# Optimization experiments

Measured on AMD Instinct MI355X. Metric: run time of the kernel, lower is better.

Reference implementation:

```python
import jax, jax.numpy as jnp
import numpy as np

B, S, D = 4, 2048, 256   # batch, seq, d_output (= d_k = d_v here)
H = 8                    # num_head


def setup_inputs() -> dict:
    key = jax.random.key(0)
    ks = jax.random.split(key, 8)
    Q = jax.random.normal(ks[0], (B, S, D), dtype=jnp.float32)
    K = jax.random.normal(ks[1], (B, S, D), dtype=jnp.float32)
    V = jax.random.normal(ks[2], (B, S, D), dtype=jnp.float32)
    M = jax.random.uniform(ks[3], (B, S, S), dtype=jnp.float32)  # multiplicative mask
    # per-head projection weights, stacked over heads (truncated_normal ~ normal here)
    W_Q = jax.random.normal(ks[4], (H, D, D), dtype=jnp.float32) * 0.05
    W_K = jax.random.normal(ks[5], (H, D, D), dtype=jnp.float32) * 0.05
    W_V = jax.random.normal(ks[6], (H, D, D), dtype=jnp.float32) * 0.05
    W_mh = jax.random.normal(ks[7], (H * D, D), dtype=jnp.float32) * 0.05
    return {"Q": Q, "K": K, "V": V, "M": M,
            "W_Q": W_Q, "W_K": W_K, "W_V": W_V, "W_mh": W_mh}


def reference(Q, K, V, M, W_Q, W_K, W_V, W_mh):
    d_k = W_Q.shape[-1]
    scale = 1.0 / np.sqrt(d_k).astype(np.float32)
    # per-head projections, vectorized over heads
    Qh = jnp.einsum('bsd,hdk->bhsk', Q, W_Q)          # [B,H,S,dk]
    Kh = jnp.einsum('bsd,hdk->bhsk', K, W_K)          # [B,H,S,dk]
    Vh = jnp.einsum('bsd,hdv->bhsv', V, W_V)          # [B,H,S,dv]
    # scaled similarity with MULTIPLICATIVE mask applied before softmax
    scores = jnp.einsum('bhsk,bhtk->bhst', Qh, Kh) * scale * M[:, None]
    attn = jax.nn.softmax(scores, axis=-1)            # [B,H,S,S]
    heads = jnp.einsum('bhst,bhtv->bhsv', attn, Vh)   # [B,H,S,dv]
    # concat heads along feature dim: [B,S,H*dv]
    Bv, Hv, Sv, Dv = heads.shape
    heads = heads.transpose(0, 2, 1, 3).reshape(Bv, Sv, Hv * Dv)
    return heads @ W_mh                               # [B,S,d_output]
```

## Files before the change

kernel.cpp:

```cpp
#include <hip/hip_runtime.h>
#include <hip/hip_bf16.h>
#include <stdint.h>

#define B_ 4
#define S_ 2048
#define D_ 256
#define H_ 8

using f32x4  = __attribute__((ext_vector_type(4))) float;
using f32x16 = __attribute__((ext_vector_type(16))) float;
using bf16x4 = __attribute__((ext_vector_type(4))) __bf16;
using bf16x8 = __attribute__((ext_vector_type(8))) __bf16;

static __device__ __forceinline__ unsigned short f2bf(float x) {
    union { float f; unsigned u; } v; v.f = x;
    unsigned r = (v.u + 0x7FFFu + ((v.u >> 16) & 1u)) >> 16;
    return (unsigned short)r;
}

static __device__ __forceinline__ f32x4 mfma16(bf16x8 a, bf16x8 b, f32x4 c) {
    return __builtin_amdgcn_mfma_f32_16x16x32_bf16(a, b, c, 0, 0, 0);
}
static __device__ __forceinline__ f32x16 mfma32(bf16x8 a, bf16x8 b, f32x16 c) {
    return __builtin_amdgcn_mfma_f32_32x32x16_bf16(a, b, c, 0, 0, 0);
}

static __device__ __forceinline__ unsigned cvt_pk_bf16(float lo, float hi) {
    unsigned r;
    asm volatile("v_cvt_pk_bf16_f32 %0, %1, %2" : "=v"(r) : "v"(lo), "v"(hi));
    return r;
}

static __device__ __forceinline__ void gl_lds16(const void* g, void* l) {
    __builtin_amdgcn_global_load_lds((const __attribute__((address_space(1))) void*)g,
                                     (__attribute__((address_space(3))) void*)l, 16, 0, 0);
}
static __device__ __forceinline__ void gl_lds4(const void* g, void* l) {
    __builtin_amdgcn_global_load_lds((const __attribute__((address_space(1))) void*)g,
                                     (__attribute__((address_space(3))) void*)l, 4, 0, 0);
}

static __device__ __forceinline__ void drain_vmem_then_sync() {
    asm volatile("s_waitcnt vmcnt(0)" ::: "memory");
    __builtin_amdgcn_sched_barrier(0);
    __syncthreads();
}

__global__ __launch_bounds__(256) void wtrans_kernel(
        const float* __restrict__ Wq, const float* __restrict__ Wk,
        const float* __restrict__ Wv, const float* __restrict__ Wmh,
        unsigned short* __restrict__ WqkvT, unsigned short* __restrict__ WmhT) {
    int idx = blockIdx.x * 256 + threadIdx.x;
    const int NQKV = 3 * H_ * 256 * 256;
    if (idx < NQKV) {
        int d = idx & 255, n = (idx >> 8) & 255, h = (idx >> 16) & 7, which = idx >> 19;
        const float* W = (which == 0) ? Wq : ((which == 1) ? Wk : Wv);
        WqkvT[idx] = f2bf(W[(h * 256 + d) * 256 + n]);
    } else {
        int j = idx - NQKV;
        int k = j & 2047, n = j >> 11;
        WmhT[j] = f2bf(Wmh[k * 256 + n]);
    }
}

__global__ __launch_bounds__(256, 2) void proj_kernel(
        const float* __restrict__ Q, const float* __restrict__ K,
        const float* __restrict__ V, const unsigned short* __restrict__ WqkvT,
        unsigned short* __restrict__ Qh, unsigned short* __restrict__ Kh,
        unsigned short* __restrict__ VhT) {
    __shared__ __attribute__((aligned(16))) unsigned char smem[65536];
    int tid = threadIdx.x;
    int nt = blockIdx.x & 3, h = (blockIdx.x >> 2) & 7, which = blockIdx.x >> 5;
    int mt = blockIdx.y;
    const float* X = (which == 0) ? Q : ((which == 1) ? K : V);

    {
        const float4* Xv = (const float4*)(X + (size_t)mt * 64 * 256);
        #pragma unroll
        for (int j = 0; j < 16; ++j) {
            int c = tid + 256 * j;
            int row = c >> 6, c4 = c & 63;
            float4 x = Xv[c];
            ushort4 p;
            p.x = f2bf(x.x); p.y = f2bf(x.y); p.z = f2bf(x.z); p.w = f2bf(x.w);
            *(ushort4*)(smem + row * 512 + ((c4 * 8) ^ ((row & 7) << 4))) = p;
        }
    }
    {
        const uint4* Wv_ = (const uint4*)(WqkvT + (size_t)((which * H_ + h) * 256 + nt * 64) * 256);
        #pragma unroll
        for (int j = 0; j < 8; ++j) {
            int c = tid + 256 * j;
            int row = c >> 5, slot = c & 31;
            *(uint4*)(smem + 32768 + row * 512 + ((slot * 16) ^ ((row & 7) << 4))) = Wv_[c];
        }
    }
    __syncthreads();

    int w = tid >> 6, l = tid & 63, lr = l & 15, lg = l >> 4;
    f32x4 acc[4];
    #pragma unroll
    for (int fr = 0; fr < 4; ++fr) acc[fr] = (f32x4){0.f, 0.f, 0.f, 0.f};

    #pragma unroll
    for (int ks = 0; ks < 8; ++ks) {
        int arow = 16 * w + lr;
        bf16x8 a = *(const bf16x8*)(smem + arow * 512 + ((64 * ks + 16 * lg) ^ ((arow & 7) << 4)));
        #pragma unroll
        for (int fr = 0; fr < 4; ++fr) {
            int brow = 16 * fr + lr;
            bf16x8 b = *(const bf16x8*)(smem + 32768 + brow * 512 + ((64 * ks + 16 * lg) ^ ((brow & 7) << 4)));
            acc[fr] = mfma16(a, b, acc[fr]);
        }
    }

    int m0 = mt * 64 + 16 * w + 4 * lg;
    int b = m0 >> 11, s0 = m0 & 2047;
    if (which < 2) {
        unsigned short* out = (which == 0) ? Qh : Kh;
        float sc = (which == 0) ? 0.0625f : 1.0f;
        #pragma unroll
        for (int fr = 0; fr < 4; ++fr) {
            int n = nt * 64 + 16 * fr + lr;
            #pragma unroll
            for (int i = 0; i < 4; ++i)
                out[(size_t)((b * H_ + h) * S_ + s0 + i) * D_ + n] = f2bf(acc[fr][i] * sc);
        }
    } else {
        #pragma unroll
        for (int fr = 0; fr < 4; ++fr) {
            int n = nt * 64 + 16 * fr + lr;
            ushort4 p;
            p.x = f2bf(acc[fr][0]); p.y = f2bf(acc[fr][1]);
            p.z = f2bf(acc[fr][2]); p.w = f2bf(acc[fr][3]);
            *(ushort4*)(VhT + (size_t)((b * H_ + h) * D_ + n) * S_ + s0) = p;
        }
    }
}

__global__ __launch_bounds__(512, 2) void attn2_kernel(
        const unsigned short* Qh, const unsigned short* __restrict__ Kh,
        const unsigned short* __restrict__ VhT, const float* __restrict__ M,
        unsigned short* heads) {
    __shared__ __attribute__((aligned(16))) unsigned char smem[131072];
    const int tid = threadIdx.x;
    const int w = tid >> 6, l = tid & 63;
    const int qg = w >> 1, ts = w & 1;
    const int ql = l & 31, hi = l >> 5;

    int n = blockIdx.x;
    int x = n & 7, r0 = n >> 3;
    int h = r0 & 7, ghi = r0 >> 3;
    int g = x + 8 * ghi;
    int qt = g & 15, b = g >> 4;
    int bh = b * H_ + h;

    const unsigned short* KhP = Kh + (size_t)bh * S_ * D_;
    const unsigned short* VTP = VhT + (size_t)bh * D_ * S_;

    const int q = qt * 128 + qg * 32 + ql;
    const float* MrowP = M + (size_t)b * S_ * S_ + (size_t)q * S_;

    bf16x8 qf[16];
    {
        const unsigned short* QhP = Qh + ((size_t)bh * S_ + q) * D_;
        #pragma unroll
        for (int ks = 0; ks < 16; ++ks)
            qf[ks] = *(const bf16x8*)(QhP + ks * 16 + hi * 8);
    }

    f32x16 o[8];
    #pragma unroll
    for (int vb = 0; vb < 8; ++vb) o[vb] = (f32x16){};
    float mrun = -1e30f, lrun = 0.f;

    const int krow = ts * 32 + ql;
    const unsigned kbase = (unsigned)(krow * 512 + ((hi * 16) ^ ((krow & 15) << 5)));
    const unsigned vtbase = (unsigned)(ql * 128 + (((ts * 64) | (hi * 16)) ^ ((ql & 15) << 3)));

    const int ksr = 8 * w + (l >> 5);
    const unsigned kcol = (l & 31) * 16;
    const int vsr = 32 * w + (l >> 5);
    const unsigned vcol = (l & 31) * 4;

    int cur = 0;

    auto stage = [&](int tt, int bsel) {
        unsigned char* kb = smem + bsel * 32768;
        unsigned char* vb = smem + 65536 + bsel * 32768;
        #pragma unroll
        for (int j = 0; j < 4; ++j) {
            int row = ksr + 2 * j;
            const unsigned char* src = (const unsigned char*)KhP +
                (size_t)(tt * 64 + row) * 512 + (kcol ^ ((row & 15) << 5));
            gl_lds16(src, kb + (8 * w + 2 * j) * 512);
        }
        #pragma unroll
        for (int i = 0; i < 16; ++i) {
            int v = vsr + 2 * i;
            const unsigned char* src = (const unsigned char*)VTP +
                (size_t)v * (S_ * 2) + tt * 128 + (vcol ^ ((v & 15) << 3));
            gl_lds4(src, vb + (32 * w + 2 * i) * 128);
        }
    };

    stage(0, 0);
    drain_vmem_then_sync();

    #pragma unroll 1
    for (int tt = 0; tt < 32; ++tt) {
        stage((tt + 1) & 31, cur ^ 1);

        const unsigned char* kp = smem + cur * 32768;
        const unsigned char* vp = smem + 65536 + cur * 32768;

        const float* Mt = MrowP + tt * 64 + ts * 32 + 4 * hi;
        float4 mv0 = *(const float4*)(Mt);
        float4 mv1 = *(const float4*)(Mt + 8);
        float4 mv2 = *(const float4*)(Mt + 16);
        float4 mv3 = *(const float4*)(Mt + 24);

        f32x16 sacc = (f32x16){};
        #pragma unroll
        for (int ks = 0; ks < 16; ++ks) {
            bf16x8 a = *(const bf16x8*)(kp + (kbase ^ (unsigned)(ks * 32)));
            sacc = mfma32(a, qf[ks], sacc);
        }

        float p[16];
        #pragma unroll
        for (int rg = 0; rg < 4; ++rg) {
            float4 mv = (rg == 0) ? mv0 : (rg == 1) ? mv1 : (rg == 2) ? mv2 : mv3;
            #pragma unroll
            for (int j = 0; j < 4; ++j) p[4 * rg + j] = sacc[4 * rg + j] * ((const float*)&mv)[j];
        }

        float tm = p[0];
        #pragma unroll
        for (int i = 1; i < 16; ++i) tm = fmaxf(tm, p[i]);
        float tmm = fmaxf(tm, __shfl_xor(tm, 32, 64));

        if (__any(tmm > mrun)) {
            float nm = fmaxf(mrun, tmm);
            float f = __expf(mrun - nm);
            #pragma unroll
            for (int vb = 0; vb < 8; ++vb) o[vb] *= f;
            lrun *= f;
            mrun = nm;
        }

        float rs = 0.f;
        #pragma unroll
        for (int i = 0; i < 16; ++i) { p[i] = __expf(p[i] - mrun); rs += p[i]; }
        lrun += rs;

        unsigned own0 = cvt_pk_bf16(p[0], p[1]),  own1 = cvt_pk_bf16(p[2], p[3]);
        unsigned own2 = cvt_pk_bf16(p[4], p[5]),  own3 = cvt_pk_bf16(p[6], p[7]);
        unsigned own4 = cvt_pk_bf16(p[8], p[9]),  own5 = cvt_pk_bf16(p[10], p[11]);
        unsigned own6 = cvt_pk_bf16(p[12], p[13]), own7 = cvt_pk_bf16(p[14], p[15]);
        unsigned rec0 = __shfl_xor((int)own0, 32, 64), rec1 = __shfl_xor((int)own1, 32, 64);
        unsigned rec2 = __shfl_xor((int)own2, 32, 64), rec3 = __shfl_xor((int)own3, 32, 64);
        unsigned rec4 = __shfl_xor((int)own4, 32, 64), rec5 = __shfl_xor((int)own5, 32, 64);
        unsigned rec6 = __shfl_xor((int)own6, 32, 64), rec7 = __shfl_xor((int)own7, 32, 64);

        union { unsigned u[4]; bf16x8 v; } f0, f1;
        f0.u[0] = hi ? rec2 : own0;  f0.u[1] = hi ? rec3 : own1;
        f0.u[2] = hi ? own2 : rec0;  f0.u[3] = hi ? own3 : rec1;
        f1.u[0] = hi ? rec6 : own4;  f1.u[1] = hi ? rec7 : own5;
        f1.u[2] = hi ? own6 : rec4;  f1.u[3] = hi ? own7 : rec5;

        #pragma unroll
        for (int tstep = 0; tstep < 2; ++tstep) {
            bf16x8 pf = tstep ? f1.v : f0.v;
            unsigned a0 = vtbase ^ (unsigned)(tstep * 32);
            #pragma unroll
            for (int vb = 0; vb < 8; ++vb) {
                bf16x4 lo4 = *(const bf16x4*)(vp + vb * 4096 + a0);
                bf16x4 hi4 = *(const bf16x4*)(vp + vb * 4096 + (a0 ^ 8u));
                bf16x8 av = __builtin_shufflevector(lo4, hi4, 0, 1, 2, 3, 4, 5, 6, 7);
                o[vb] = mfma32(av, pf, o[vb]);
            }
        }

        drain_vmem_then_sync();
        cur ^= 1;
    }

    lrun += __shfl_xor(lrun, 32, 64);

    float2* mlb = (float2*)smem;
    if (hi == 0) mlb[(qg * 2 + ts) * 32 + ql] = make_float2(mrun, lrun);
    __syncthreads();
    float2 oth = mlb[(qg * 2 + (ts ^ 1)) * 32 + ql];
    __syncthreads();

    float mstar = fmaxf(mrun, oth.x);
    float aS = __expf(mrun - mstar), aO = __expf(oth.x - mstar);
    float inv = 1.f / (aS * lrun + aO * oth.y);
    float sc = aS * inv;
    #pragma unroll
    for (int vb = 0; vb < 8; ++vb) o[vb] *= sc;

    float* ob = (float*)smem;
    if (ts == 1) {
        #pragma unroll
        for (int vb = 0; vb < 8; ++vb)
            #pragma unroll
            for (int r = 0; r < 16; ++r) {
                int v = 32 * vb + (r & 3) + 8 * (r >> 2) + 4 * hi;
                ob[qg * 8192 + v * 32 + ql] = o[vb][r];
            }
    }
    __syncthreads();
    if (ts == 0) {
        unsigned short* hp = heads + ((size_t)bh * S_ + q) * D_;
        #pragma unroll
        for (int vb = 0; vb < 8; ++vb) {
            #pragma unroll
            for (int rg = 0; rg < 4; ++rg) {
                int v0 = 32 * vb + 8 * rg + 4 * hi;
                ushort4 pk;
                pk.x = f2bf(o[vb][4 * rg + 0] + ob[qg * 8192 + (v0 + 0) * 32 + ql]);
                pk.y = f2bf(o[vb][4 * rg + 1] + ob[qg * 8192 + (v0 + 1) * 32 + ql]);
                pk.z = f2bf(o[vb][4 * rg + 2] + ob[qg * 8192 + (v0 + 2) * 32 + ql]);
                pk.w = f2bf(o[vb][4 * rg + 3] + ob[qg * 8192 + (v0 + 3) * 32 + ql]);
                *(ushort4*)(hp + v0) = pk;
            }
        }
    }
}

__global__ __launch_bounds__(256, 2) void out_kernel(
        const unsigned short* __restrict__ heads,
        const unsigned short* __restrict__ WmhT, float* __restrict__ out) {
    __shared__ __attribute__((aligned(16))) unsigned char smem[65536];
    int tid = threadIdx.x;
    int nt = blockIdx.x, mt = blockIdx.y;
    int w = tid >> 6, l = tid & 63, lr = l & 15, lg = l >> 4;
    int m0 = mt * 64;
    int b = m0 >> 11, s00 = m0 & 2047;

    f32x4 acc[4];
    #pragma unroll
    for (int fr = 0; fr < 4; ++fr) acc[fr] = (f32x4){0.f, 0.f, 0.f, 0.f};

    for (int h = 0; h < H_; ++h) {
        __syncthreads();
        {
            const uint4* src = (const uint4*)(heads + (size_t)((b * H_ + h) * S_ + s00) * D_);
            #pragma unroll
            for (int j = 0; j < 8; ++j) {
                int c = tid + 256 * j;
                int row = c >> 5, slot = c & 31;
                *(uint4*)(smem + row * 512 + ((slot * 16) ^ ((row & 7) << 4))) = src[c];
            }
        }
        {
            #pragma unroll
            for (int j = 0; j < 8; ++j) {
                int c = tid + 256 * j;
                int row = c >> 5, slot = c & 31;
                uint4 xx = *(const uint4*)(WmhT + (size_t)(nt * 64 + row) * 2048 + h * 256 + slot * 8);
                *(uint4*)(smem + 32768 + row * 512 + ((slot * 16) ^ ((row & 7) << 4))) = xx;
            }
        }
        __syncthreads();
        #pragma unroll
        for (int ks = 0; ks < 8; ++ks) {
            int arow = 16 * w + lr;
            bf16x8 a = *(const bf16x8*)(smem + arow * 512 + ((64 * ks + 16 * lg) ^ ((arow & 7) << 4)));
            #pragma unroll
            for (int fr = 0; fr < 4; ++fr) {
                int brow = 16 * fr + lr;
                bf16x8 bb = *(const bf16x8*)(smem + 32768 + brow * 512 + ((64 * ks + 16 * lg) ^ ((brow & 7) << 4)));
                acc[fr] = mfma16(a, bb, acc[fr]);
            }
        }
    }

    int mrow = mt * 64 + 16 * w + 4 * lg;
    #pragma unroll
    for (int fr = 0; fr < 4; ++fr) {
        int nn = nt * 64 + 16 * fr + lr;
        #pragma unroll
        for (int i = 0; i < 4; ++i)
            out[(size_t)(mrow + i) * D_ + nn] = acc[fr][i];
    }
}

extern "C" void kernel_launch(void* const* d_in, const int* in_sizes, int n_in,
                              void* d_out, int out_size, void* d_ws, size_t ws_size,
                              hipStream_t stream) {
    const float* Q   = (const float*)d_in[0];
    const float* K   = (const float*)d_in[1];
    const float* V   = (const float*)d_in[2];
    const float* M   = (const float*)d_in[3];
    const float* Wq  = (const float*)d_in[4];
    const float* Wk  = (const float*)d_in[5];
    const float* Wv  = (const float*)d_in[6];
    const float* Wmh = (const float*)d_in[7];
    float* out = (float*)d_out;

    char* ws = (char*)d_ws;
    unsigned short* Qh    = (unsigned short*)(ws);
    unsigned short* Kh    = (unsigned short*)(ws + 33554432);
    unsigned short* VhT   = (unsigned short*)(ws + 67108864);
    unsigned short* WqkvT = (unsigned short*)(ws + 100663296);
    unsigned short* WmhT  = (unsigned short*)(ws + 103809024);

    wtrans_kernel<<<dim3(8192), dim3(256), 0, stream>>>(Wq, Wk, Wv, Wmh, WqkvT, WmhT);
    proj_kernel<<<dim3(96, 128), dim3(256), 0, stream>>>(Q, K, V, WqkvT, Qh, Kh, VhT);
    attn2_kernel<<<dim3(512), dim3(512), 0, stream>>>(Qh, Kh, VhT, M, Qh);
    out_kernel<<<dim3(4, 128), dim3(256), 0, stream>>>(Qh, WmhT, out);
}
```

Before: 644.0 us.

## Pre-convert mask to bf16, prefetch mask tiles, lazy softmax rescale, reorder blocks

```diff
diff --git a/kernel.cpp b/kernel.cpp
--- a/kernel.cpp
+++ b/kernel.cpp
@@ -16,6 +16,10 @@
     union { float f; unsigned u; } v; v.f = x;
     unsigned r = (v.u + 0x7FFFu + ((v.u >> 16) & 1u)) >> 16;
     return (unsigned short)r;
+}
+static __device__ __forceinline__ float bf2f(unsigned short u) {
+    union { unsigned u32; float f; } v; v.u32 = ((unsigned)u) << 16;
+    return v.f;
 }
 
 static __device__ __forceinline__ f32x4 mfma16(bf16x8 a, bf16x8 b, f32x4 c) {
@@ -63,6 +67,18 @@
     }
 }
 
+__global__ __launch_bounds__(256) void mconv_kernel(
+        const float* __restrict__ M, unsigned short* __restrict__ Mb) {
+    int i = (blockIdx.x * 256 + threadIdx.x) * 8;
+    float4 a = *(const float4*)(M + i);
+    float4 b = *(const float4*)(M + i + 4);
+    ushort4 lo, hi;
+    lo.x = f2bf(a.x); lo.y = f2bf(a.y); lo.z = f2bf(a.z); lo.w = f2bf(a.w);
+    hi.x = f2bf(b.x); hi.y = f2bf(b.y); hi.z = f2bf(b.z); hi.w = f2bf(b.w);
+    *(ushort4*)(Mb + i) = lo;
+    *(ushort4*)(Mb + i + 4) = hi;
+}
+
 __global__ __launch_bounds__(256, 2) void proj_kernel(
         const float* __restrict__ Q, const float* __restrict__ K,
         const float* __restrict__ V, const unsigned short* __restrict__ WqkvT,
@@ -138,10 +154,11 @@
     }
 }
 
+template <bool MB>
 __global__ __launch_bounds__(512, 2) void attn2_kernel(
         const unsigned short* Qh, const unsigned short* __restrict__ Kh,
         const unsigned short* __restrict__ VhT, const float* __restrict__ M,
-        unsigned short* heads) {
+        const unsigned short* __restrict__ Mb, unsigned short* heads) {
     __shared__ __attribute__((aligned(16))) unsigned char smem[131072];
     const int tid = threadIdx.x;
     const int w = tid >> 6, l = tid & 63;
@@ -149,17 +166,15 @@
     const int ql = l & 31, hi = l >> 5;
 
     int n = blockIdx.x;
-    int x = n & 7, r0 = n >> 3;
-    int h = r0 & 7, ghi = r0 >> 3;
-    int g = x + 8 * ghi;
-    int qt = g & 15, b = g >> 4;
+    int h = n & 7, qt = (n >> 3) & 15, b = n >> 7;
     int bh = b * H_ + h;
 
     const unsigned short* KhP = Kh + (size_t)bh * S_ * D_;
     const unsigned short* VTP = VhT + (size_t)bh * D_ * S_;
 
     const int q = qt * 128 + qg * 32 + ql;
-    const float* MrowP = M + (size_t)b * S_ * S_ + (size_t)q * S_;
+    const float* MP = M + (size_t)b * S_ * S_ + (size_t)q * S_;
+    const unsigned short* MbP = Mb + (size_t)b * S_ * S_ + (size_t)q * S_;
 
     bf16x8 qf[16];
     {
@@ -204,7 +219,26 @@
         }
     };
 
+    ushort4 mh0, mh1, mh2, mh3;
+    float4  mf0, mf1, mf2, mf3;
+    auto mload = [&](int tt) {
+        if constexpr (MB) {
+            const unsigned short* p = MbP + tt * 64 + ts * 32 + 4 * hi;
+            mh0 = *(const ushort4*)(p);
+            mh1 = *(const ushort4*)(p + 8);
+            mh2 = *(const ushort4*)(p + 16);
+            mh3 = *(const ushort4*)(p + 24);
+        } else {
+            const float* p = MP + tt * 64 + ts * 32 + 4 * hi;
+            mf0 = *(const float4*)(p);
+            mf1 = *(const float4*)(p + 8);
+            mf2 = *(const float4*)(p + 16);
+            mf3 = *(const float4*)(p + 24);
+        }
+    };
+
     stage(0, 0);
+    mload(0);
     drain_vmem_then_sync();
 
     #pragma unroll 1
@@ -214,12 +248,6 @@
         const unsigned char* kp = smem + cur * 32768;
         const unsigned char* vp = smem + 65536 + cur * 32768;
 
-        const float* Mt = MrowP + tt * 64 + ts * 32 + 4 * hi;
-        float4 mv0 = *(const float4*)(Mt);
-        float4 mv1 = *(const float4*)(Mt + 8);
-        float4 mv2 = *(const float4*)(Mt + 16);
-        float4 mv3 = *(const float4*)(Mt + 24);
-
         f32x16 sacc = (f32x16){};
         #pragma unroll
         for (int ks = 0; ks < 16; ++ks) {
@@ -228,19 +256,34 @@
         }
 
         float p[16];
-        #pragma unroll
-        for (int rg = 0; rg < 4; ++rg) {
-            float4 mv = (rg == 0) ? mv0 : (rg == 1) ? mv1 : (rg == 2) ? mv2 : mv3;
-            #pragma unroll
-            for (int j = 0; j < 4; ++j) p[4 * rg + j] = sacc[4 * rg + j] * ((const float*)&mv)[j];
-        }
+        if constexpr (MB) {
+            p[0]  = sacc[0]  * bf2f(mh0.x); p[1]  = sacc[1]  * bf2f(mh0.y);
+            p[2]  = sacc[2]  * bf2f(mh0.z); p[3]  = sacc[3]  * bf2f(mh0.w);
+            p[4]  = sacc[4]  * bf2f(mh1.x); p[5]  = sacc[5]  * bf2f(mh1.y);
+            p[6]  = sacc[6]  * bf2f(mh1.z); p[7]  = sacc[7]  * bf2f(mh1.w);
+            p[8]  = sacc[8]  * bf2f(mh2.x); p[9]  = sacc[9]  * bf2f(mh2.y);
+            p[10] = sacc[10] * bf2f(mh2.z); p[11] = sacc[11] * bf2f(mh2.w);
+            p[12] = sacc[12] * bf2f(mh3.x); p[13] = sacc[13] * bf2f(mh3.y);
+            p[14] = sacc[14] * bf2f(mh3.z); p[15] = sacc[15] * bf2f(mh3.w);
+        } else {
+            p[0]  = sacc[0]  * mf0.x; p[1]  = sacc[1]  * mf0.y;
+            p[2]  = sacc[2]  * mf0.z; p[3]  = sacc[3]  * mf0.w;
+            p[4]  = sacc[4]  * mf1.x; p[5]  = sacc[5]  * mf1.y;
+            p[6]  = sacc[6]  * mf1.z; p[7]  = sacc[7]  * mf1.w;
+            p[8]  = sacc[8]  * mf2.x; p[9]  = sacc[9]  * mf2.y;
+            p[10] = sacc[10] * mf2.z; p[11] = sacc[11] * mf2.w;
+            p[12] = sacc[12] * mf3.x; p[13] = sacc[13] * mf3.y;
+            p[14] = sacc[14] * mf3.z; p[15] = sacc[15] * mf3.w;
+        }
+
+        mload((tt + 1) & 31);
 
         float tm = p[0];
         #pragma unroll
         for (int i = 1; i < 16; ++i) tm = fmaxf(tm, p[i]);
         float tmm = fmaxf(tm, __shfl_xor(tm, 32, 64));
 
-        if (__any(tmm > mrun)) {
+        if (__any(tmm > mrun + 8.0f)) {
             float nm = fmaxf(mrun, tmm);
             float f = __expf(mrun - nm);
             #pragma unroll
@@ -407,9 +450,17 @@
     unsigned short* VhT   = (unsigned short*)(ws + 67108864);
     unsigned short* WqkvT = (unsigned short*)(ws + 100663296);
     unsigned short* WmhT  = (unsigned short*)(ws + 103809024);
-
+    unsigned short* Mb    = (unsigned short*)(ws + 104857600);
+
+    const bool useMb = ws_size >= (size_t)104857600 + 33554432;
+
+    if (useMb)
+        mconv_kernel<<<dim3(8192), dim3(256), 0, stream>>>(M, Mb);
     wtrans_kernel<<<dim3(8192), dim3(256), 0, stream>>>(Wq, Wk, Wv, Wmh, WqkvT, WmhT);
     proj_kernel<<<dim3(96, 128), dim3(256), 0, stream>>>(Q, K, V, WqkvT, Qh, Kh, VhT);
-    attn2_kernel<<<dim3(512), dim3(512), 0, stream>>>(Qh, Kh, VhT, M, Qh);
+    if (useMb)
+        attn2_kernel<true><<<dim3(512), dim3(512), 0, stream>>>(Qh, Kh, VhT, M, Mb, Qh);
+    else
+        attn2_kernel<false><<<dim3(512), dim3(512), 0, stream>>>(Qh, Kh, VhT, M, Mb, Qh);
     out_kernel<<<dim3(4, 128), dim3(256), 0, stream>>>(Qh, WmhT, out);
 }
```

Measured after the change: 653.3 us. About the same (+1.4%).
